# Performance work log

Measured on AMD Instinct MI355X. Metric: run time of the kernel, lower is better.

## Reference

```python
import jax, jax.numpy as jnp
import numpy as np

B, T, F = 32, 64, 128          # batch, time_steps, input_dim
H = 8                           # feat_dim (GRU hidden, MHA embed)
NH, HD = 4, 2                   # num_heads, head_dim
HID = 32                        # hidden_dim (out_proj out-features)


def setup_inputs() -> dict:
    key = jax.random.key(0)
    ks = jax.random.split(key, 16)
    s = 0.1
    inp = {
        'x': jax.random.normal(ks[0], (B, T, F), jnp.float32),
        # input_proj: Linear(F, F)
        'Wp': jax.random.normal(ks[1], (F, F), jnp.float32) * s,
        'bp': jax.random.normal(ks[2], (F,), jnp.float32) * s,
        # per-feature GRU weights stacked over F (input size 1 -> squeeze)
        'W_ih': jax.random.normal(ks[3], (F, 3 * H), jnp.float32) * s,
        'b_ih': jax.random.normal(ks[4], (F, 3 * H), jnp.float32) * s,
        'W_hh': jax.random.normal(ks[5], (F, 3 * H, H), jnp.float32) * s,
        'b_hh': jax.random.normal(ks[6], (F, 3 * H), jnp.float32) * s,
        # shared MultiheadAttention (embed=H, heads=NH)
        'in_w': jax.random.normal(ks[7], (3 * H, H), jnp.float32) * s,
        'in_b': jax.random.normal(ks[8], (3 * H,), jnp.float32) * s,
        'ow': jax.random.normal(ks[9], (H, H), jnp.float32) * s,
        'ob': jax.random.normal(ks[10], (H,), jnp.float32) * s,
        # out_proj: Linear(F*H, HID)
        'Wout': jax.random.normal(ks[11], (HID, F * H), jnp.float32) * s,
        'bout': jax.random.normal(ks[12], (HID,), jnp.float32) * s,
    }
    return inp


def _forward(x, Wp, bp, W_ih, b_ih, W_hh, b_hh, in_w, in_b, ow, ob, Wout, bout):
    xp = x @ Wp.T + bp                               # [B,T,F] input_proj

    # ---- batched per-feature GRU (vectorized over B and F, scan over T) ----
    def step(h, x_t):                                # h [B,F,H], x_t [B,F]
        gx = x_t[..., None] * W_ih + b_ih            # [B,F,3H]
        gh = jnp.einsum('bfh,fgh->bfg', h, W_hh) + b_hh
        r = jax.nn.sigmoid(gx[..., :H] + gh[..., :H])
        z = jax.nn.sigmoid(gx[..., H:2 * H] + gh[..., H:2 * H])
        n = jnp.tanh(gx[..., 2 * H:] + r * gh[..., 2 * H:])
        h_new = (1.0 - z) * n + z * h
        return h_new, h_new

    h0 = jnp.zeros((x.shape[0], F, H), x.dtype)
    _, hs = jax.lax.scan(step, h0, jnp.moveaxis(xp, 1, 0))   # [T,B,F,H]
    out = jnp.moveaxis(hs, 0, 1)                              # [B,T,F,H]

    # ---- shared MHA over time, batched across (B, F) ----
    seq = out.transpose(0, 2, 1, 3)                           # [B,F,T,H]
    qkv = seq @ in_w.T + in_b                                 # [B,F,T,3H]
    q, k, v = jnp.split(qkv, 3, axis=-1)
    def heads(t):  # [B,F,T,H] -> [B,F,T,NH,HD]
        return t.reshape(t.shape[:-1] + (NH, HD))
    q, k, v = heads(q), heads(k), heads(v)
    scale = 1.0 / np.sqrt(HD)
    scores = jnp.einsum('bfqnd,bfknd->bfnqk', q, k) * scale   # [B,F,NH,T,T]
    w = jax.nn.softmax(scores, axis=-1)
    ctx = jnp.einsum('bfnqk,bfknd->bfqnd', w, v)
    ctx = ctx.reshape(ctx.shape[:2] + (ctx.shape[2], H))      # [B,F,T,H]
    attn_out = ctx @ ow.T + ob                                # [B,F,T,H]
    attention = attn_out.transpose(0, 2, 1, 3)                # [B,T,F,H]

    # ---- flatten GRU outputs and project ----
    y = out.reshape(out.shape[0], out.shape[1], F * H) @ Wout.T + bout  # [B,T,HID]
    return y, attention


def reference(x, Wp, bp, W_ih, b_ih, W_hh, b_hh, in_w, in_b, ow, ob, Wout, bout):
    return _forward(x, Wp, bp, W_ih, b_ih, W_hh, b_hh, in_w, in_b, ow, ob, Wout, bout)
```

## Files before the change

### kernel.cpp

```cpp
#include <hip/hip_runtime.h>


namespace {
constexpr int Bb = 32, Tt = 64, Ff = 128, Hh = 8, HIDh = 32;
constexpr int G3H = 24;
constexpr float L2E = 1.44269504088896340736f;
constexpr int XS_STRIDE = 130;
constexpr int XP = 8320;
constexpr int OCT = 4160;
constexpr int WKV = 9280;
constexpr int KK0 = 0, KK1 = 272, VV0 = 544, VV1 = 816, QS = 1088;
constexpr int SM_SIZE = 16192;
}

__device__ __forceinline__ float rcp_(float x) {
#if __has_builtin(__builtin_amdgcn_rcpf)
  return __builtin_amdgcn_rcpf(x);
#else
  return 1.0f / x;
#endif
}
__device__ __forceinline__ float exp2_(float x) {
#if __has_builtin(__builtin_amdgcn_exp2f)
  return __builtin_amdgcn_exp2f(x);
#else
  return exp2f(x);
#endif
}

#define MHA_STEP(K0C, K1C, V0C, V1C)                         \
  {                                                          \
    _Pragma("unroll") for (int i = 0; i < 4; ++i) {          \
      float s = fmaf(q0[i], K0C, q1[i] * K1C);               \
      float p = exp2_(s);                                    \
      ps[i] += p;                                            \
      c0[i] = fmaf(p, V0C, c0[i]);                           \
      c1[i] = fmaf(p, V1C, c1[i]);                           \
    }                                                        \
  }

__global__ __launch_bounds__(256, 2) void k_fused(
    const float* __restrict__ x, const float* __restrict__ Wp, const float* __restrict__ bp,
    const float* __restrict__ W_ih, const float* __restrict__ b_ih,
    const float* __restrict__ W_hh, const float* __restrict__ b_hh,
    const float* __restrict__ in_w, const float* __restrict__ in_b,
    const float* __restrict__ ow, const float* __restrict__ ob,
    float* __restrict__ outp, float* __restrict__ attn) {
  __shared__ float smem[SM_SIZE];
  const int tid = threadIdx.x;
  const int blk = blockIdx.x;
  const int b = blk >> 4;
  const int f0 = (blk & 15) * 8;
  const int lane = tid & 63;
  const int w = tid >> 6;

  {
    const float2* xb = (const float2*)(x + b * Tt * Ff);
    for (int i = tid; i < Tt * Ff / 2; i += 256) {
      int row = i >> 6, col2 = i & 63;
      *(float2*)&smem[row * XS_STRIDE + col2 * 2] = xb[i];
    }
  }
  __syncthreads();
  {
    const int t = lane;
    const int fA = f0 + w, fB = f0 + w + 4;
    float acc0 = bp[fA], acc1 = bp[fB];
    const float* wA = Wp + fA * Ff;
    const float* wB = Wp + fB * Ff;
    const float* xr = &smem[t * XS_STRIDE];
#pragma unroll 8
    for (int k = 0; k < Ff; k += 2) {
      float2 xv = *(const float2*)&xr[k];
      acc0 = fmaf(xv.x, wA[k], acc0); acc0 = fmaf(xv.y, wA[k + 1], acc0);
      acc1 = fmaf(xv.x, wB[k], acc1); acc1 = fmaf(xv.y, wB[k + 1], acc1);
    }
    smem[XP + w * 65 + t] = acc0;
    smem[XP + (w + 4) * 65 + t] = acc1;
  }
  __syncthreads();

  if (tid < 64) {
    __builtin_amdgcn_s_setprio(1);
    const int g = tid >> 3, j = tid & 7;
    const int f = f0 + g;
    const float* wb = W_hh + (f * G3H + j) * Hh;
    const float nL = -L2E, S2 = 2.0f * L2E;
    float w0s[8], w1s[8], w2s[8];
#pragma unroll
    for (int h = 0; h < 8; ++h) {
      w0s[h] = wb[h] * nL;
      w1s[h] = wb[64 + h] * nL;
      w2s[h] = wb[128 + h] * S2;
    }
    const float wi0s = W_ih[f * G3H + j] * nL;
    const float wi1s = W_ih[f * G3H + 8 + j] * nL;
    const float wi2s = W_ih[f * G3H + 16 + j] * S2;
    const float bias_r = (b_ih[f * G3H + j] + b_hh[f * G3H + j]) * nL;
    const float bias_z = (b_ih[f * G3H + 8 + j] + b_hh[f * G3H + 8 + j]) * nL;
    const float bi2s = b_ih[f * G3H + 16 + j] * S2;
    const float bh2s = b_hh[f * G3H + 16 + j] * S2;
    float hall[8];
#pragma unroll
    for (int h = 0; h < 8; ++h) hall[h] = 0.f;
    const int base = tid & 56;
    float* hdst = &smem[g * 520 + j * 65];
    const float* xps = &smem[XP + g * 65];
    for (int t = 0; t < Tt; ++t) {
      float xt = xps[t];
      float a0 = bias_r, a1 = bias_z, a2 = bh2s;
#pragma unroll
      for (int h = 0; h < 8; ++h) {
        a0 = fmaf(hall[h], w0s[h], a0);
        a1 = fmaf(hall[h], w1s[h], a1);
        a2 = fmaf(hall[h], w2s[h], a2);
      }
      float r = rcp_(1.0f + exp2_(fmaf(xt, wi0s, a0)));
      float z = rcp_(1.0f + exp2_(fmaf(xt, wi1s, a1)));
      float narg = fmaf(r, a2, fmaf(xt, wi2s, bi2s));
      float n = fmaf(-2.0f, rcp_(exp2_(narg) + 1.0f), 1.0f);
      float hn = fmaf(z, hall[j] - n, n);
      hdst[t] = hn;
#pragma unroll
      for (int h = 0; h < 8; ++h) hall[h] = __shfl(hn, base + h, 64);
    }
    __builtin_amdgcn_s_setprio(0);
  }
  __syncthreads();

  {
    float4* og = (float4*)(outp + (b * Ff + f0) * Tt * Hh);
#pragma unroll
    for (int i = 0; i < 4; ++i) {
      int v = i * 256 + tid;
      int g = v >> 7;
      int rem = v & 127;
      int t = rem >> 1, j0 = (rem & 1) * 4;
      const float* hp = &smem[g * 520 + j0 * 65 + t];
      og[v] = make_float4(hp[0], hp[65], hp[130], hp[195]);
    }
  }

  {
    const int t = lane;
    float* sm = &smem[WKV + w * 1728];
    constexpr float SCL = 0.70710678118654752f * L2E;
#pragma unroll
    for (int fl = w; fl < 8; fl += 4) {
      const float* hsrc = &smem[fl * 520];
      float sq[8];
#pragma unroll
      for (int h = 0; h < 8; ++h) sq[h] = hsrc[h * 65 + t];
      float qv[8], ka[8], va[8];
#pragma unroll
      for (int jj = 0; jj < 8; ++jj) {
        float aq = in_b[jj], ak = in_b[8 + jj], av = in_b[16 + jj];
#pragma unroll
        for (int h = 0; h < 8; ++h) {
          aq = fmaf(sq[h], in_w[jj * 8 + h], aq);
          ak = fmaf(sq[h], in_w[(8 + jj) * 8 + h], ak);
          av = fmaf(sq[h], in_w[(16 + jj) * 8 + h], av);
        }
        qv[jj] = aq * SCL; ka[jj] = ak; va[jj] = av;
      }
#pragma unroll
      for (int n = 0; n < 4; ++n) {
        *(float2*)&sm[QS + t * 10 + 2 * n] = make_float2(qv[2 * n], qv[2 * n + 1]);
        sm[KK0 + n * 68 + t] = ka[2 * n];
        sm[KK1 + n * 68 + t] = ka[2 * n + 1];
        sm[VV0 + n * 68 + t] = va[2 * n];
        sm[VV1 + n * 68 + t] = va[2 * n + 1];
      }
      asm volatile("s_waitcnt lgkmcnt(0)" ::: "memory");

      const int n = t >> 4, qq = t & 15;
      float q0[4], q1[4];
#pragma unroll
      for (int i = 0; i < 4; ++i) {
        float2 qp = *(const float2*)&sm[QS + (qq + 16 * i) * 10 + 2 * n];
        q0[i] = qp.x; q1[i] = qp.y;
      }
      float ps[4], c0[4], c1[4];
#pragma unroll
      for (int i = 0; i < 4; ++i) { ps[i] = 0.f; c0[i] = 0.f; c1[i] = 0.f; }
#pragma unroll 2
      for (int kt4 = 0; kt4 < Tt; kt4 += 4) {
        float4 k0 = *(const float4*)&sm[KK0 + n * 68 + kt4];
        float4 k1 = *(const float4*)&sm[KK1 + n * 68 + kt4];
        float4 v0 = *(const float4*)&sm[VV0 + n * 68 + kt4];
        float4 v1 = *(const float4*)&sm[VV1 + n * 68 + kt4];
        MHA_STEP(k0.x, k1.x, v0.x, v1.x)
        MHA_STEP(k0.y, k1.y, v0.y, v1.y)
        MHA_STEP(k0.z, k1.z, v0.z, v1.z)
        MHA_STEP(k0.w, k1.w, v0.w, v1.w)
      }
#pragma unroll
      for (int i = 0; i < 4; ++i) {
        float inv = rcp_(ps[i]);
        *(float2*)&sm[QS + (qq + 16 * i) * 10 + 2 * n] =
            make_float2(c0[i] * inv, c1[i] * inv);
      }
      asm volatile("s_waitcnt lgkmcnt(0)" ::: "memory");

      {
        float2 cp0 = *(const float2*)&sm[QS + t * 10 + 0];
        float2 cp1 = *(const float2*)&sm[QS + t * 10 + 2];
        float2 cp2 = *(const float2*)&sm[QS + t * 10 + 4];
        float2 cp3 = *(const float2*)&sm[QS + t * 10 + 6];
        float cx[8] = {cp0.x, cp0.y, cp1.x, cp1.y, cp2.x, cp2.y, cp3.x, cp3.y};
        float o8[8];
#pragma unroll
        for (int jj = 0; jj < 8; ++jj) {
          float a = ob[jj];
#pragma unroll
          for (int h = 0; h < 8; ++h) a = fmaf(cx[h], ow[jj * 8 + h], a);
          o8[jj] = a;
        }
        float* od = &smem[OCT + fl * 640 + t * 10];
        *(float4*)&od[0] = make_float4(o8[0], o8[1], o8[2], o8[3]);
        *(float4*)&od[4] = make_float4(o8[4], o8[5], o8[6], o8[7]);
      }
    }
  }
  __syncthreads();

  {
#pragma unroll
    for (int i = 0; i < 4; ++i) {
      int v = i * 256 + tid;
      int t = v >> 4;
      int c = v & 15;
      const float* sp = &smem[OCT + (c >> 1) * 640 + t * 10 + (c & 1) * 4];
      float4* dst = (float4*)(attn + ((b * Tt + t) * Ff + f0) * Hh);
      dst[v & 15 ? c : c] = *(const float4*)sp;
    }
  }
}

__global__ __launch_bounds__(128) void k_outproj(
    const float* __restrict__ outp, const float* __restrict__ Wout,
    const float* __restrict__ bout, float* __restrict__ y) {
  constexpr int TT = 8;
  int blk = blockIdx.x;
  int b = blk >> 3;
  int t0 = (blk & 7) * TT;
  int tid = threadIdx.x;
  int oq = tid >> 4;
  int fc = tid & 15;
  float acc[TT][4];
#pragma unroll
  for (int tt = 0; tt < TT; ++tt)
#pragma unroll
    for (int od = 0; od < 4; ++od) acc[tt][od] = 0.f;
#pragma unroll
  for (int ff = 0; ff < 8; ++ff) {
    int f = fc * 8 + ff;
    const float4* rb = (const float4*)(outp + ((b * Ff + f) * Tt + t0) * Hh);
    float4 rv[16];
#pragma unroll
    for (int i = 0; i < 16; ++i) rv[i] = rb[i];
#pragma unroll
    for (int od = 0; od < 4; ++od) {
      int o = oq * 4 + od;
      const float4* wbp = (const float4*)(Wout + o * (Ff * Hh) + f * Hh);
      float4 wa = wbp[0], wc = wbp[1];
#pragma unroll
      for (int tt = 0; tt < TT; ++tt) {
        float4 ra = rv[tt * 2], rc = rv[tt * 2 + 1];
        float s = acc[tt][od];
        s = fmaf(ra.x, wa.x, s); s = fmaf(ra.y, wa.y, s);
        s = fmaf(ra.z, wa.z, s); s = fmaf(ra.w, wa.w, s);
        s = fmaf(rc.x, wc.x, s); s = fmaf(rc.y, wc.y, s);
        s = fmaf(rc.z, wc.z, s); s = fmaf(rc.w, wc.w, s);
        acc[tt][od] = s;
      }
    }
  }
#pragma unroll
  for (int tt = 0; tt < TT; ++tt)
#pragma unroll
    for (int od = 0; od < 4; ++od) {
      float v = acc[tt][od];
      v += __shfl_xor(v, 1, 16);
      v += __shfl_xor(v, 2, 16);
      v += __shfl_xor(v, 4, 16);
      v += __shfl_xor(v, 8, 16);
      acc[tt][od] = v;
    }
#pragma unroll
  for (int tt = 0; tt < TT; ++tt) {
    if (fc == tt) {
#pragma unroll
      for (int od = 0; od < 4; ++od) {
        int o = oq * 4 + od;
        y[(b * Tt + t0 + tt) * HIDh + o] = acc[tt][od] + bout[o];
      }
    }
  }
}

extern "C" void kernel_launch(void* const* d_in, const int* in_sizes, int n_in,
                              void* d_out, int out_size, void* d_ws, size_t ws_size,
                              hipStream_t stream) {
  (void)in_sizes; (void)n_in; (void)out_size; (void)ws_size;
  const float* x    = (const float*)d_in[0];
  const float* Wp   = (const float*)d_in[1];
  const float* bp   = (const float*)d_in[2];
  const float* W_ih = (const float*)d_in[3];
  const float* b_ih = (const float*)d_in[4];
  const float* W_hh = (const float*)d_in[5];
  const float* b_hh = (const float*)d_in[6];
  const float* in_w = (const float*)d_in[7];
  const float* in_b = (const float*)d_in[8];
  const float* ow   = (const float*)d_in[9];
  const float* ob   = (const float*)d_in[10];
  const float* Wout = (const float*)d_in[11];
  const float* bout = (const float*)d_in[12];

  float* y    = (float*)d_out;
  float* attn = (float*)d_out + Bb * Tt * HIDh;
  float* outp = (float*)d_ws;

  hipLaunchKernelGGL(k_fused, dim3(Bb * (Ff / 8)), dim3(256), 0, stream,
                     x, Wp, bp, W_ih, b_ih, W_hh, b_hh, in_w, in_b, ow, ob, outp, attn);
  hipLaunchKernelGGL(k_outproj, dim3(Bb * (Tt / 8)), dim3(128), 0, stream,
                     outp, Wout, bout, y);
}
```

Before: 56.89 us.

## Split fused GRU+MHA kernel into single-wave blocks of two features each

The fused kernel now launches 2048 single-wavefront blocks, each handling two features, instead of 512 four-wave blocks handling eight. This removes block-level barriers in favour of LDS waitcnts, reads x and Wp directly from global memory rather than staging x in shared memory, and uses a compact t-major hidden-state layout that is reused in place for Q, context and output. The aim is more parallel recurrences across CUs and less shared memory per block. In exchange, only 16 of 64 lanes do the GRU recurrence, and each block re-reads its x rows from global.

```diff
diff --git a/kernel.cpp b/kernel.cpp
--- a/kernel.cpp
+++ b/kernel.cpp
@@ -5,12 +5,12 @@
 constexpr int Bb = 32, Tt = 64, Ff = 128, Hh = 8, HIDh = 32;
 constexpr int G3H = 24;
 constexpr float L2E = 1.44269504088896340736f;
-constexpr int XS_STRIDE = 130;
-constexpr int XP = 8320;
-constexpr int OCT = 4160;
-constexpr int WKV = 9280;
-constexpr int KK0 = 0, KK1 = 272, VV0 = 544, VV1 = 816, QS = 1088;
-constexpr int SM_SIZE = 16192;
+constexpr int XPS = 0;
+constexpr int UB  = 132;
+constexpr int UBS = 772;
+constexpr int KV  = 132 + 2 * 772;
+constexpr int KK0 = KV, KK1 = KV + 272, VV0 = KV + 544, VV1 = KV + 816;
+constexpr int SM_SIZE = KV + 1088;
 }
 
 __device__ __forceinline__ float rcp_(float x) {
@@ -39,7 +39,7 @@
     }                                                        \
   }
 
-__global__ __launch_bounds__(256, 2) void k_fused(
+__global__ __launch_bounds__(64) void k_fused(
     const float* __restrict__ x, const float* __restrict__ Wp, const float* __restrict__ bp,
     const float* __restrict__ W_ih, const float* __restrict__ b_ih,
     const float* __restrict__ W_hh, const float* __restrict__ b_hh,
@@ -47,42 +47,32 @@
     const float* __restrict__ ow, const float* __restrict__ ob,
     float* __restrict__ outp, float* __restrict__ attn) {
   __shared__ float smem[SM_SIZE];
-  const int tid = threadIdx.x;
+  const int t = threadIdx.x;
   const int blk = blockIdx.x;
-  const int b = blk >> 4;
-  const int f0 = (blk & 15) * 8;
-  const int lane = tid & 63;
-  const int w = tid >> 6;
+  const int b = blk >> 6;
+  const int f0 = (blk & 63) * 2;
 
   {
-    const float2* xb = (const float2*)(x + b * Tt * Ff);
-    for (int i = tid; i < Tt * Ff / 2; i += 256) {
-      int row = i >> 6, col2 = i & 63;
-      *(float2*)&smem[row * XS_STRIDE + col2 * 2] = xb[i];
-    }
-  }
-  __syncthreads();
-  {
-    const int t = lane;
-    const int fA = f0 + w, fB = f0 + w + 4;
-    float acc0 = bp[fA], acc1 = bp[fB];
-    const float* wA = Wp + fA * Ff;
-    const float* wB = Wp + fB * Ff;
-    const float* xr = &smem[t * XS_STRIDE];
+    const float4* xr = (const float4*)(x + (b * Tt + t) * Ff);
+    const float4* wA = (const float4*)(Wp + f0 * Ff);
+    const float4* wB = (const float4*)(Wp + (f0 + 1) * Ff);
+    float a0 = bp[f0], a1 = bp[f0 + 1];
 #pragma unroll 8
-    for (int k = 0; k < Ff; k += 2) {
-      float2 xv = *(const float2*)&xr[k];
-      acc0 = fmaf(xv.x, wA[k], acc0); acc0 = fmaf(xv.y, wA[k + 1], acc0);
-      acc1 = fmaf(xv.x, wB[k], acc1); acc1 = fmaf(xv.y, wB[k + 1], acc1);
-    }
-    smem[XP + w * 65 + t] = acc0;
-    smem[XP + (w + 4) * 65 + t] = acc1;
-  }
-  __syncthreads();
-
-  if (tid < 64) {
+    for (int k = 0; k < Ff / 4; ++k) {
+      float4 xv = xr[k], va = wA[k], vb = wB[k];
+      a0 = fmaf(xv.x, va.x, a0); a0 = fmaf(xv.y, va.y, a0);
+      a0 = fmaf(xv.z, va.z, a0); a0 = fmaf(xv.w, va.w, a0);
+      a1 = fmaf(xv.x, vb.x, a1); a1 = fmaf(xv.y, vb.y, a1);
+      a1 = fmaf(xv.z, vb.z, a1); a1 = fmaf(xv.w, vb.w, a1);
+    }
+    smem[XPS + t] = a0;
+    smem[XPS + 65 + t] = a1;
+  }
+  asm volatile("s_waitcnt lgkmcnt(0)" ::: "memory");
+
+  if (t < 16) {
     __builtin_amdgcn_s_setprio(1);
-    const int g = tid >> 3, j = tid & 7;
+    const int g = t >> 3, j = t & 7;
     const int f = f0 + g;
     const float* wb = W_hh + (f * G3H + j) * Hh;
     const float nL = -L2E, S2 = 2.0f * L2E;
@@ -103,11 +93,12 @@
     float hall[8];
 #pragma unroll
     for (int h = 0; h < 8; ++h) hall[h] = 0.f;
-    const int base = tid & 56;
-    float* hdst = &smem[g * 520 + j * 65];
-    const float* xps = &smem[XP + g * 65];
-    for (int t = 0; t < Tt; ++t) {
-      float xt = xps[t];
+    float h_own = 0.f;
+    const int base = t & 56;
+    float* hdst = &smem[UB + g * UBS + j];
+    const float* xps = &smem[XPS + g * 65];
+    for (int tt = 0; tt < Tt; ++tt) {
+      float xt = xps[tt];
       float a0 = bias_r, a1 = bias_z, a2 = bh2s;
 #pragma unroll
       for (int h = 0; h < 8; ++h) {
@@ -119,65 +110,64 @@
       float z = rcp_(1.0f + exp2_(fmaf(xt, wi1s, a1)));
       float narg = fmaf(r, a2, fmaf(xt, wi2s, bi2s));
       float n = fmaf(-2.0f, rcp_(exp2_(narg) + 1.0f), 1.0f);
-      float hn = fmaf(z, hall[j] - n, n);
-      hdst[t] = hn;
+      float hn = fmaf(z, h_own - n, n);
+      hdst[tt * 12] = hn;
+      h_own = hn;
 #pragma unroll
       for (int h = 0; h < 8; ++h) hall[h] = __shfl(hn, base + h, 64);
     }
     __builtin_amdgcn_s_setprio(0);
   }
-  __syncthreads();
+  asm volatile("s_waitcnt lgkmcnt(0)" ::: "memory");
 
   {
     float4* og = (float4*)(outp + (b * Ff + f0) * Tt * Hh);
 #pragma unroll
     for (int i = 0; i < 4; ++i) {
-      int v = i * 256 + tid;
-      int g = v >> 7;
-      int rem = v & 127;
-      int t = rem >> 1, j0 = (rem & 1) * 4;
-      const float* hp = &smem[g * 520 + j0 * 65 + t];
-      og[v] = make_float4(hp[0], hp[65], hp[130], hp[195]);
-    }
-  }
-
-  {
-    const int t = lane;
-    float* sm = &smem[WKV + w * 1728];
-    constexpr float SCL = 0.70710678118654752f * L2E;
-#pragma unroll
-    for (int fl = w; fl < 8; fl += 4) {
-      const float* hsrc = &smem[fl * 520];
-      float sq[8];
-#pragma unroll
-      for (int h = 0; h < 8; ++h) sq[h] = hsrc[h * 65 + t];
-      float qv[8], ka[8], va[8];
-#pragma unroll
-      for (int jj = 0; jj < 8; ++jj) {
-        float aq = in_b[jj], ak = in_b[8 + jj], av = in_b[16 + jj];
-#pragma unroll
-        for (int h = 0; h < 8; ++h) {
-          aq = fmaf(sq[h], in_w[jj * 8 + h], aq);
-          ak = fmaf(sq[h], in_w[(8 + jj) * 8 + h], ak);
-          av = fmaf(sq[h], in_w[(16 + jj) * 8 + h], av);
-        }
-        qv[jj] = aq * SCL; ka[jj] = ak; va[jj] = av;
-      }
-#pragma unroll
-      for (int n = 0; n < 4; ++n) {
-        *(float2*)&sm[QS + t * 10 + 2 * n] = make_float2(qv[2 * n], qv[2 * n + 1]);
-        sm[KK0 + n * 68 + t] = ka[2 * n];
-        sm[KK1 + n * 68 + t] = ka[2 * n + 1];
-        sm[VV0 + n * 68 + t] = va[2 * n];
-        sm[VV1 + n * 68 + t] = va[2 * n + 1];
-      }
-      asm volatile("s_waitcnt lgkmcnt(0)" ::: "memory");
-
+      int v = i * 64 + t;
+      int fl = v >> 7, rem = v & 127;
+      int tt = rem >> 1, j0 = (rem & 1) * 4;
+      og[v] = *(const float4*)&smem[UB + fl * UBS + tt * 12 + j0];
+    }
+  }
+  asm volatile("s_waitcnt lgkmcnt(0)" ::: "memory");
+
+  constexpr float SCL = 0.70710678118654752f * L2E;
+#pragma unroll
+  for (int fl = 0; fl < 2; ++fl) {
+    float* ub = &smem[UB + fl * UBS];
+    float sq[8];
+    *(float4*)&sq[0] = *(const float4*)&ub[t * 12];
+    *(float4*)&sq[4] = *(const float4*)&ub[t * 12 + 4];
+    float qv[8], ka[8], va[8];
+#pragma unroll
+    for (int jj = 0; jj < 8; ++jj) {
+      float aq = in_b[jj], ak = in_b[8 + jj], av = in_b[16 + jj];
+#pragma unroll
+      for (int h = 0; h < 8; ++h) {
+        aq = fmaf(sq[h], in_w[jj * 8 + h], aq);
+        ak = fmaf(sq[h], in_w[(8 + jj) * 8 + h], ak);
+        av = fmaf(sq[h], in_w[(16 + jj) * 8 + h], av);
+      }
+      qv[jj] = aq * SCL; ka[jj] = ak; va[jj] = av;
+    }
+    *(float4*)&ub[t * 12] = make_float4(qv[0], qv[1], qv[2], qv[3]);
+    *(float4*)&ub[t * 12 + 4] = make_float4(qv[4], qv[5], qv[6], qv[7]);
+#pragma unroll
+    for (int n = 0; n < 4; ++n) {
+      smem[KK0 + n * 68 + t] = ka[2 * n];
+      smem[KK1 + n * 68 + t] = ka[2 * n + 1];
+      smem[VV0 + n * 68 + t] = va[2 * n];
+      smem[VV1 + n * 68 + t] = va[2 * n + 1];
+    }
+    asm volatile("s_waitcnt lgkmcnt(0)" ::: "memory");
+
+    {
       const int n = t >> 4, qq = t & 15;
       float q0[4], q1[4];
 #pragma unroll
       for (int i = 0; i < 4; ++i) {
-        float2 qp = *(const float2*)&sm[QS + (qq + 16 * i) * 10 + 2 * n];
+        float2 qp = *(const float2*)&ub[(qq + 16 * i) * 12 + 2 * n];
         q0[i] = qp.x; q1[i] = qp.y;
       }
       float ps[4], c0[4], c1[4];
@@ -185,10 +175,10 @@
       for (int i = 0; i < 4; ++i) { ps[i] = 0.f; c0[i] = 0.f; c1[i] = 0.f; }
 #pragma unroll 2
       for (int kt4 = 0; kt4 < Tt; kt4 += 4) {
-        float4 k0 = *(const float4*)&sm[KK0 + n * 68 + kt4];
-        float4 k1 = *(const float4*)&sm[KK1 + n * 68 + kt4];
-        float4 v0 = *(const float4*)&sm[VV0 + n * 68 + kt4];
-        float4 v1 = *(const float4*)&sm[VV1 + n * 68 + kt4];
+        float4 k0 = *(const float4*)&smem[KK0 + n * 68 + kt4];
+        float4 k1 = *(const float4*)&smem[KK1 + n * 68 + kt4];
+        float4 v0 = *(const float4*)&smem[VV0 + n * 68 + kt4];
+        float4 v1 = *(const float4*)&smem[VV1 + n * 68 + kt4];
         MHA_STEP(k0.x, k1.x, v0.x, v1.x)
         MHA_STEP(k0.y, k1.y, v0.y, v1.y)
         MHA_STEP(k0.z, k1.z, v0.z, v1.z)
@@ -197,42 +187,38 @@
 #pragma unroll
       for (int i = 0; i < 4; ++i) {
         float inv = rcp_(ps[i]);
-        *(float2*)&sm[QS + (qq + 16 * i) * 10 + 2 * n] =
+        *(float2*)&ub[(qq + 16 * i) * 12 + 2 * n] =
             make_float2(c0[i] * inv, c1[i] * inv);
       }
-      asm volatile("s_waitcnt lgkmcnt(0)" ::: "memory");
-
-      {
-        float2 cp0 = *(const float2*)&sm[QS + t * 10 + 0];
-        float2 cp1 = *(const float2*)&sm[QS + t * 10 + 2];
-        float2 cp2 = *(const float2*)&sm[QS + t * 10 + 4];
-        float2 cp3 = *(const float2*)&sm[QS + t * 10 + 6];
-        float cx[8] = {cp0.x, cp0.y, cp1.x, cp1.y, cp2.x, cp2.y, cp3.x, cp3.y};
-        float o8[8];
-#pragma unroll
-        for (int jj = 0; jj < 8; ++jj) {
-          float a = ob[jj];
-#pragma unroll
-          for (int h = 0; h < 8; ++h) a = fmaf(cx[h], ow[jj * 8 + h], a);
-          o8[jj] = a;
-        }
-        float* od = &smem[OCT + fl * 640 + t * 10];
-        *(float4*)&od[0] = make_float4(o8[0], o8[1], o8[2], o8[3]);
-        *(float4*)&od[4] = make_float4(o8[4], o8[5], o8[6], o8[7]);
-      }
-    }
-  }
-  __syncthreads();
+    }
+    asm volatile("s_waitcnt lgkmcnt(0)" ::: "memory");
+
+    {
+      float cx[8];
+      *(float4*)&cx[0] = *(const float4*)&ub[t * 12];
+      *(float4*)&cx[4] = *(const float4*)&ub[t * 12 + 4];
+      float o8[8];
+#pragma unroll
+      for (int jj = 0; jj < 8; ++jj) {
+        float a = ob[jj];
+#pragma unroll
+        for (int h = 0; h < 8; ++h) a = fmaf(cx[h], ow[jj * 8 + h], a);
+        o8[jj] = a;
+      }
+      *(float4*)&ub[t * 12] = make_float4(o8[0], o8[1], o8[2], o8[3]);
+      *(float4*)&ub[t * 12 + 4] = make_float4(o8[4], o8[5], o8[6], o8[7]);
+    }
+    asm volatile("s_waitcnt lgkmcnt(0)" ::: "memory");
+  }
 
   {
 #pragma unroll
     for (int i = 0; i < 4; ++i) {
-      int v = i * 256 + tid;
-      int t = v >> 4;
-      int c = v & 15;
-      const float* sp = &smem[OCT + (c >> 1) * 640 + t * 10 + (c & 1) * 4];
-      float4* dst = (float4*)(attn + ((b * Tt + t) * Ff + f0) * Hh);
-      dst[v & 15 ? c : c] = *(const float4*)sp;
+      int v = i * 64 + t;
+      int tt = v >> 2, c = v & 3;
+      int fl = c >> 1, h0 = (c & 1) * 4;
+      float4 val = *(const float4*)&smem[UB + fl * UBS + tt * 12 + h0];
+      *(float4*)(attn + ((b * Tt + tt) * Ff + f0 + fl) * Hh + h0) = val;
     }
   }
 }
@@ -321,7 +307,7 @@
   float* attn = (float*)d_out + Bb * Tt * HIDh;
   float* outp = (float*)d_ws;
 
-  hipLaunchKernelGGL(k_fused, dim3(Bb * (Ff / 8)), dim3(256), 0, stream,
+  hipLaunchKernelGGL(k_fused, dim3(Bb * (Ff / 2)), dim3(64), 0, stream,
                      x, Wp, bp, W_ih, b_ih, W_hh, b_hh, in_w, in_b, ow, ob, outp, attn);
   hipLaunchKernelGGL(k_outproj, dim3(Bb * (Tt / 8)), dim3(128), 0, stream,
                      outp, Wout, bout, y);
```

After: 64.97 us. +14.2%, slower.
